# Kernel tuning notes

Hardware: AMD Instinct MI355X
Metric: run time of the kernel (lower is better)

The kernel has to match this reference:

```python
import jax, jax.numpy as jnp
import numpy as np
import math

N = 100000
D = 128      # input_dim
H = 4        # heads
DK = 32      # d_k
DV = D // H  # d_v = 32


def setup_inputs() -> dict:
    key = jax.random.key(0)
    k1, k2, k3, k4, k5 = jax.random.split(key, 5)
    x = jax.random.normal(k1, (N, D), dtype=jnp.float32)
    neighbor_index = jax.random.randint(k2, (N, 4), 0, N, dtype=jnp.int64)
    w_q = jax.random.normal(k3, (H, D, DK), dtype=jnp.float32) * 0.05
    w_k = jax.random.normal(k4, (H, 5, D, DK), dtype=jnp.float32) * 0.05
    w_v = jax.random.normal(k5, (H, 5, D, DV), dtype=jnp.float32) * 0.05
    return {"x": x, "neighbor_index": neighbor_index, "w_q": w_q, "w_k": w_k, "w_v": w_v}


def reference(x, neighbor_index, w_q, w_k, w_v):
    n = x.shape[0]
    d_k = w_q.shape[-1]
    # gather 4 neighbors, prepend self node -> (N, 5, D)
    x_neighbors = jnp.concatenate([x[:, None, :], x[neighbor_index]], axis=1)
    Q = jnp.einsum('nd,hdk->hnk', x, w_q)                 # (H, N, DK)
    K = jnp.einsum('nrd,hrdk->hnrk', x_neighbors, w_k)    # (H, N, 5, DK)
    V = jnp.einsum('nrd,hrdv->hnrv', x_neighbors, w_v)    # (H, N, 5, DV)
    A = jnp.einsum('hnk,hnrk->hnr', Q, K) / math.sqrt(d_k)
    # NOTE: original torch code applies softmax over dim=1, which is the NODE
    # dimension (not the neighbor dimension r). Replicated faithfully.
    A = jax.nn.softmax(A, axis=1)
    Z = jnp.einsum('hnr,hnrv->hnv', A, V)                 # (H, N, DV)
    return Z.transpose(1, 0, 2).reshape(n, -1)            # (N, H*DV)
```

## Files before the change

### kernel.cpp

```cpp
#include <hip/hip_runtime.h>


#define N_NODES 100000
#define D 128
#define H 4
#define R 5
#define NPB 64
#define THREADS 256
#define NBLOCKS ((N_NODES + NPB - 1) / NPB)

typedef _Float16 half_t;
typedef __attribute__((ext_vector_type(8))) _Float16 f16x8;
typedef __attribute__((ext_vector_type(4))) float f32x4;

typedef const __attribute__((address_space(1))) unsigned int* gp_t;
typedef __attribute__((address_space(3))) unsigned int* lp_t;

__device__ __forceinline__ void async_copy16(const void* g, void* l) {
    __builtin_amdgcn_global_load_lds((gp_t)g, (lp_t)l, 16, 0, 0);
}

__global__ void prep_x(const float* __restrict__ x, half_t* __restrict__ xh)
{
    const int total = N_NODES * D / 8;
    for (int i = blockIdx.x * blockDim.x + threadIdx.x; i < total;
         i += gridDim.x * blockDim.x) {
        const float4* s = (const float4*)x + (size_t)i * 2;
        float4 a = s[0], b = s[1];
        f16x8 h = {(half_t)a.x, (half_t)a.y, (half_t)a.z, (half_t)a.w,
                   (half_t)b.x, (half_t)b.y, (half_t)b.z, (half_t)b.w};
        *((f16x8*)xh + i) = h;
    }
}

__global__ void prep_w(const float* __restrict__ wq, const float* __restrict__ wk,
                       const float* __restrict__ wv, half_t* __restrict__ wph)
{
    const int m = blockIdx.x;
    const float* src = (m < 4) ? (wq + m * 4096)
                     : (m < 24) ? (wk + (m - 4) * 4096)
                                : (wv + (m - 24) * 4096);
    const int t = threadIdx.x;
#pragma unroll
    for (int i = 0; i < 16; ++i) {
        int p = t * 16 + i;
        int j = p & 7, ln = (p >> 3) & 63, f = p >> 9;
        int kt = f & 3, mt = f >> 2;
        int d = kt * 32 + (ln >> 4) * 8 + j;
        int ko = mt * 16 + (ln & 15);
        wph[m * 4096 + p] = (half_t)src[d * 32 + ko];
    }
}

__device__ __forceinline__ void stage_tile(const half_t* __restrict__ xh,
                                           const int* __restrict__ nbr,
                                           int base, int r, char* tile)
{
    const int w = threadIdx.x >> 6;
    const int lane = threadIdx.x & 63;
    const int rr = lane >> 4, c = lane & 15;
#pragma unroll
    for (int i = 0; i < 4; ++i) {
        int row0 = w * 16 + i * 4;
        int row = row0 + rr;
        int node = base + row;
        if (node >= N_NODES) node = N_NODES - 1;
        int src = (r == 0) ? node : nbr[node * 4 + (r - 1)];
        const char* g = (const char*)xh + (size_t)src * 256 + ((c ^ (row & 7)) << 4);
        async_copy16(g, tile + row0 * 256);
    }
}

__device__ __forceinline__ void proj(int mid, const half_t* __restrict__ wph,
                                     const half_t* tile, int lane,
                                     f32x4 (&acc)[2][4])
{
    const int l15 = lane & 15;
    const int q = lane >> 4;
#pragma unroll
    for (int mt = 0; mt < 2; ++mt)
#pragma unroll
        for (int nt = 0; nt < 4; ++nt)
            acc[mt][nt] = (f32x4){0.f, 0.f, 0.f, 0.f};

#pragma unroll
    for (int kt = 0; kt < 4; ++kt) {
        f16x8 a0 = *(const f16x8*)(wph + ((mid * 8 + kt) * 64 + lane) * 8);
        f16x8 a1 = *(const f16x8*)(wph + ((mid * 8 + 4 + kt) * 64 + lane) * 8);
#pragma unroll
        for (int nt = 0; nt < 4; ++nt) {
            int row = nt * 16 + l15;
            int sq = (kt * 4 + q) ^ (row & 7);
            f16x8 b = *(const f16x8*)(tile + row * 128 + sq * 8);
            acc[0][nt] = __builtin_amdgcn_mfma_f32_16x16x32_f16(a0, b, acc[0][nt], 0, 0, 0);
            acc[1][nt] = __builtin_amdgcn_mfma_f32_16x16x32_f16(a1, b, acc[1][nt], 0, 0, 0);
        }
    }
}

__global__ __launch_bounds__(THREADS, 3)
void knot_logits(const half_t* __restrict__ xh, const int* __restrict__ nbr,
                 const half_t* __restrict__ wph,
                 half_t* __restrict__ eh, float* __restrict__ sums_p)
{
    __shared__ __align__(16) char smem[NPB * 256];
    half_t* tile = (half_t*)smem;
    const int base = blockIdx.x * NPB;
    const int lane = threadIdx.x & 63;
    const int h = __builtin_amdgcn_readfirstlane((int)(threadIdx.x >> 6));
    const int l15 = lane & 15;

    stage_tile(xh, nbr, base, 0, smem);
    __syncthreads();

    f32x4 qf[2][4];
    proj(h, wph, tile, lane, qf);

    f32x4 kf[2][4];
#pragma unroll 1
    for (int r = 0; r < R; ++r) {
        if (r > 0) {
            __syncthreads();
            stage_tile(xh, nbr, base, r, smem);
            __syncthreads();
        }
        proj(4 + h * 5 + r, wph, tile, lane, kf);

        float esum = 0.f;
#pragma unroll
        for (int nt = 0; nt < 4; ++nt) {
            float p = 0.f;
#pragma unroll
            for (int mt = 0; mt < 2; ++mt)
#pragma unroll
                for (int j = 0; j < 4; ++j)
                    p += qf[mt][nt][j] * kf[mt][nt][j];
            p += __shfl_xor(p, 16, 64);
            p += __shfl_xor(p, 32, 64);
            int node = base + nt * 16 + l15;
            float e = (node < N_NODES) ? __expf(p * 0.17677669529663688f) : 0.f;
            if ((lane >> 4) == 0 && node < N_NODES)
                eh[(size_t)(h * 5 + r) * N_NODES + node] = (half_t)e;
            esum += e;
        }
        esum += __shfl_xor(esum, 1, 64);
        esum += __shfl_xor(esum, 2, 64);
        esum += __shfl_xor(esum, 4, 64);
        esum += __shfl_xor(esum, 8, 64);
        if (lane == 0)
            atomicAdd(&sums_p[(h * 5 + r) * 64 + (blockIdx.x & 63)], esum);
    }
}

__global__ void knot_reduce(const float* __restrict__ sums_p, float* __restrict__ sums)
{
    const int w = threadIdx.x >> 6;
    const int lane = threadIdx.x & 63;
#pragma unroll
    for (int i = 0; i < 5; ++i) {
        int hr = w * 5 + i;
        float v = sums_p[hr * 64 + lane];
        v += __shfl_xor(v, 1, 64);
        v += __shfl_xor(v, 2, 64);
        v += __shfl_xor(v, 4, 64);
        v += __shfl_xor(v, 8, 64);
        v += __shfl_xor(v, 16, 64);
        v += __shfl_xor(v, 32, 64);
        if (lane == 0) sums[hr] = v;
    }
}

#define VS 67
#define HS 2152
__global__ __launch_bounds__(THREADS, 3)
void knot_out(const half_t* __restrict__ xh, const int* __restrict__ nbr,
              const half_t* __restrict__ wph,
              const half_t* __restrict__ eh, const float* __restrict__ sums,
              float* __restrict__ out)
{
    __shared__ __align__(16) char smem[2 * HS * 4];
    half_t* tile = (half_t*)smem;
    const int base = blockIdx.x * NPB;
    const int lane = threadIdx.x & 63;
    const int h = __builtin_amdgcn_readfirstlane((int)(threadIdx.x >> 6));
    const int l15 = lane & 15;
    const int q = lane >> 4;

    f32x4 z[2][4];
#pragma unroll
    for (int mt = 0; mt < 2; ++mt)
#pragma unroll
        for (int nt = 0; nt < 4; ++nt)
            z[mt][nt] = (f32x4){0.f, 0.f, 0.f, 0.f};

    f32x4 vf[2][4];
#pragma unroll 1
    for (int r = 0; r < R; ++r) {
        if (r > 0) __syncthreads();
        stage_tile(xh, nbr, base, r, smem);
        __syncthreads();
        proj(24 + h * 5 + r, wph, tile, lane, vf);

        float inv = 1.0f / sums[h * 5 + r];
#pragma unroll
        for (int nt = 0; nt < 4; ++nt) {
            int node = base + nt * 16 + l15;
            if (node >= N_NODES) node = N_NODES - 1;
            float w = (float)eh[(size_t)(h * 5 + r) * N_NODES + node] * inv;
#pragma unroll
            for (int mt = 0; mt < 2; ++mt)
#pragma unroll
                for (int j = 0; j < 4; ++j)
                    z[mt][nt][j] += w * vf[mt][nt][j];
        }
    }

    __syncthreads();
    float* zt = (float*)smem;
#pragma unroll 1
    for (int pass = 0; pass < 2; ++pass) {
        if (pass) __syncthreads();
        if ((h >> 1) == pass) {
#pragma unroll
            for (int mt = 0; mt < 2; ++mt)
#pragma unroll
                for (int nt = 0; nt < 4; ++nt)
#pragma unroll
                    for (int j = 0; j < 4; ++j) {
                        int v = mt * 16 + q * 4 + j;
                        zt[(h & 1) * HS + v * VS + nt * 16 + l15] = z[mt][nt][j];
                    }
        }
        __syncthreads();
        const int row = threadIdx.x >> 2;
        const int c = threadIdx.x & 3;
        if (base + row < N_NODES) {
            float* dst = out + (size_t)(base + row) * D + pass * 64 + c * 16;
#pragma unroll
            for (int i4 = 0; i4 < 4; ++i4) {
                float4 v4;
#pragma unroll
                for (int e = 0; e < 4; ++e) {
                    int col = c * 16 + i4 * 4 + e;
                    int h2 = col >> 5, v = col & 31;
                    ((float*)&v4)[e] = zt[h2 * HS + v * VS + row];
                }
                *(float4*)(dst + i4 * 4) = v4;
            }
        }
    }
}

extern "C" void kernel_launch(void* const* d_in, const int* in_sizes, int n_in,
                              void* d_out, int out_size, void* d_ws, size_t ws_size,
                              hipStream_t stream)
{
    const float* x   = (const float*)d_in[0];
    const int*   nbr = (const int*)d_in[1];
    const float* w_q = (const float*)d_in[2];
    const float* w_k = (const float*)d_in[3];
    const float* w_v = (const float*)d_in[4];
    float* out = (float*)d_out;

    float*  sums   = (float*)d_ws;
    float*  sums_p = sums + 32;
    half_t* eh     = (half_t*)((char*)d_ws + 8192);
    half_t* wph    = (half_t*)((char*)d_ws + 4194304);
    half_t* xh     = (half_t*)((char*)d_ws + 4718592);

    hipMemsetAsync(d_ws, 0, 5248, stream);
    prep_x<<<2048, THREADS, 0, stream>>>(x, xh);
    prep_w<<<44, THREADS, 0, stream>>>(w_q, w_k, w_v, wph);
    knot_logits<<<NBLOCKS, THREADS, 0, stream>>>(xh, nbr, wph, eh, sums_p);
    knot_reduce<<<1, THREADS, 0, stream>>>(sums_p, sums);
    knot_out<<<NBLOCKS, THREADS, 0, stream>>>(xh, nbr, wph, eh, sums, out);
}
```

Baseline: 222.7 us.

## Double-buffer neighbor tiles, merge prep kernels, fold sum reduction into output kernel

Both the logits and output kernels now use two LDS buffers, so the gather of the next neighbor's rows is issued while MFMAs run on the current tile. Neighbor indices are loaded once per node as an int4, and the per-slot loop is unrolled at compile time. The two prep kernels become one launch, and the separate reduce kernel is removed by having each knot_out block reduce the partial sums itself. This cuts launches and sync stalls, at the cost of double the LDS per block (which may lower occupancy) and redundant per-block reduction work.

```diff
diff --git a/kernel.cpp b/kernel.cpp
--- a/kernel.cpp
+++ b/kernel.cpp
@@ -20,80 +20,92 @@
     __builtin_amdgcn_global_load_lds((gp_t)g, (lp_t)l, 16, 0, 0);
 }
 
-__global__ void prep_x(const float* __restrict__ x, half_t* __restrict__ xh)
-{
-    const int total = N_NODES * D / 8;
-    for (int i = blockIdx.x * blockDim.x + threadIdx.x; i < total;
-         i += gridDim.x * blockDim.x) {
-        const float4* s = (const float4*)x + (size_t)i * 2;
-        float4 a = s[0], b = s[1];
-        f16x8 h = {(half_t)a.x, (half_t)a.y, (half_t)a.z, (half_t)a.w,
-                   (half_t)b.x, (half_t)b.y, (half_t)b.z, (half_t)b.w};
-        *((f16x8*)xh + i) = h;
-    }
-}
-
-__global__ void prep_w(const float* __restrict__ wq, const float* __restrict__ wk,
-                       const float* __restrict__ wv, half_t* __restrict__ wph)
-{
-    const int m = blockIdx.x;
-    const float* src = (m < 4) ? (wq + m * 4096)
-                     : (m < 24) ? (wk + (m - 4) * 4096)
-                                : (wv + (m - 24) * 4096);
+template<int V> struct ic { static constexpr int value = V; };
+
+__global__ void prep(const float* __restrict__ x,
+                     const float* __restrict__ wq, const float* __restrict__ wk,
+                     const float* __restrict__ wv,
+                     half_t* __restrict__ xh, half_t* __restrict__ wph)
+{
+    const int bid = blockIdx.x;
     const int t = threadIdx.x;
-#pragma unroll
-    for (int i = 0; i < 16; ++i) {
-        int p = t * 16 + i;
-        int j = p & 7, ln = (p >> 3) & 63, f = p >> 9;
-        int kt = f & 3, mt = f >> 2;
-        int d = kt * 32 + (ln >> 4) * 8 + j;
-        int ko = mt * 16 + (ln & 15);
-        wph[m * 4096 + p] = (half_t)src[d * 32 + ko];
-    }
-}
-
-__device__ __forceinline__ void stage_tile(const half_t* __restrict__ xh,
-                                           const int* __restrict__ nbr,
-                                           int base, int r, char* tile)
-{
-    const int w = threadIdx.x >> 6;
-    const int lane = threadIdx.x & 63;
-    const int rr = lane >> 4, c = lane & 15;
+    if (bid < 44) {
+        const float* src = (bid < 4) ? (wq + bid * 4096)
+                         : (bid < 24) ? (wk + (bid - 4) * 4096)
+                                      : (wv + (bid - 24) * 4096);
+#pragma unroll
+        for (int i = 0; i < 16; ++i) {
+            int p = t * 16 + i;
+            int j = p & 7, ln = (p >> 3) & 63, f = p >> 9;
+            int kt = f & 3, mt = f >> 2;
+            int d = kt * 32 + (ln >> 4) * 8 + j;
+            int ko = mt * 16 + (ln & 15);
+            wph[bid * 4096 + p] = (half_t)src[d * 32 + ko];
+        }
+    } else {
+        const int total = N_NODES * D / 8;
+        const int nb = gridDim.x - 44;
+        for (int i = (bid - 44) * THREADS + t; i < total; i += nb * THREADS) {
+            const float4* s = (const float4*)x + (size_t)i * 2;
+            float4 a = s[0], b = s[1];
+            f16x8 h8 = {(half_t)a.x, (half_t)a.y, (half_t)a.z, (half_t)a.w,
+                        (half_t)b.x, (half_t)b.y, (half_t)b.z, (half_t)b.w};
+            *((f16x8*)xh + i) = h8;
+        }
+    }
+}
+
+template<int SLOT>
+__device__ __forceinline__ void stage_slot(const half_t* __restrict__ xh,
+                                           const int (&rows)[4], const int4 (&nb4)[4],
+                                           int base, char* buf, int lane)
+{
+    const int rr = lane >> 4;
+    const int c = lane & 15;
 #pragma unroll
     for (int i = 0; i < 4; ++i) {
-        int row0 = w * 16 + i * 4;
-        int row = row0 + rr;
-        int node = base + row;
-        if (node >= N_NODES) node = N_NODES - 1;
-        int src = (r == 0) ? node : nbr[node * 4 + (r - 1)];
+        int row = rows[i];
+        int src;
+        if constexpr (SLOT == 0) {
+            int node = base + row;
+            src = (node >= N_NODES) ? (N_NODES - 1) : node;
+        } else if constexpr (SLOT == 1) src = nb4[i].x;
+        else if constexpr (SLOT == 2) src = nb4[i].y;
+        else if constexpr (SLOT == 3) src = nb4[i].z;
+        else                          src = nb4[i].w;
         const char* g = (const char*)xh + (size_t)src * 256 + ((c ^ (row & 7)) << 4);
-        async_copy16(g, tile + row0 * 256);
-    }
-}
-
-__device__ __forceinline__ void proj(int mid, const half_t* __restrict__ wph,
-                                     const half_t* tile, int lane,
-                                     f32x4 (&acc)[2][4])
-{
-    const int l15 = lane & 15;
-    const int q = lane >> 4;
+        async_copy16(g, buf + (row - rr) * 256);
+    }
+}
+
+__device__ __forceinline__ void load_af(int mid, const half_t* __restrict__ wph,
+                                        int lane, f16x8 (&af)[8])
+{
+#pragma unroll
+    for (int kt = 0; kt < 4; ++kt) {
+        af[kt * 2]     = *(const f16x8*)(wph + ((mid * 8 + kt) * 64 + lane) * 8);
+        af[kt * 2 + 1] = *(const f16x8*)(wph + ((mid * 8 + 4 + kt) * 64 + lane) * 8);
+    }
+}
+
+__device__ __forceinline__ void proj_mfma(const f16x8 (&af)[8], const half_t* tile,
+                                          int lane, f32x4 (&acc)[2][4])
+{
+    const int l15 = lane & 15, q = lane >> 4;
 #pragma unroll
     for (int mt = 0; mt < 2; ++mt)
 #pragma unroll
         for (int nt = 0; nt < 4; ++nt)
             acc[mt][nt] = (f32x4){0.f, 0.f, 0.f, 0.f};
-
 #pragma unroll
     for (int kt = 0; kt < 4; ++kt) {
-        f16x8 a0 = *(const f16x8*)(wph + ((mid * 8 + kt) * 64 + lane) * 8);
-        f16x8 a1 = *(const f16x8*)(wph + ((mid * 8 + 4 + kt) * 64 + lane) * 8);
 #pragma unroll
         for (int nt = 0; nt < 4; ++nt) {
             int row = nt * 16 + l15;
             int sq = (kt * 4 + q) ^ (row & 7);
             f16x8 b = *(const f16x8*)(tile + row * 128 + sq * 8);
-            acc[0][nt] = __builtin_amdgcn_mfma_f32_16x16x32_f16(a0, b, acc[0][nt], 0, 0, 0);
-            acc[1][nt] = __builtin_amdgcn_mfma_f32_16x16x32_f16(a1, b, acc[1][nt], 0, 0, 0);
+            acc[0][nt] = __builtin_amdgcn_mfma_f32_16x16x32_f16(af[kt * 2], b, acc[0][nt], 0, 0, 0);
+            acc[1][nt] = __builtin_amdgcn_mfma_f32_16x16x32_f16(af[kt * 2 + 1], b, acc[1][nt], 0, 0, 0);
         }
     }
 }
@@ -103,28 +115,41 @@
                  const half_t* __restrict__ wph,
                  half_t* __restrict__ eh, float* __restrict__ sums_p)
 {
-    __shared__ __align__(16) char smem[NPB * 256];
-    half_t* tile = (half_t*)smem;
+    __shared__ __align__(16) char bufA[NPB * 256];
+    __shared__ __align__(16) char bufB[NPB * 256];
     const int base = blockIdx.x * NPB;
     const int lane = threadIdx.x & 63;
     const int h = __builtin_amdgcn_readfirstlane((int)(threadIdx.x >> 6));
-    const int l15 = lane & 15;
-
-    stage_tile(xh, nbr, base, 0, smem);
+    const int l15 = lane & 15, rr = lane >> 4;
+
+    int rows[4]; int4 nb4[4];
+#pragma unroll
+    for (int i = 0; i < 4; ++i) {
+        rows[i] = h * 16 + i * 4 + rr;
+        int node = base + rows[i];
+        if (node >= N_NODES) node = N_NODES - 1;
+        nb4[i] = ((const int4*)nbr)[node];
+    }
+
+    stage_slot<0>(xh, rows, nb4, base, bufA, lane);
+    stage_slot<1>(xh, rows, nb4, base, bufB, lane);
     __syncthreads();
 
-    f32x4 qf[2][4];
-    proj(h, wph, tile, lane, qf);
-
-    f32x4 kf[2][4];
-#pragma unroll 1
-    for (int r = 0; r < R; ++r) {
-        if (r > 0) {
-            __syncthreads();
-            stage_tile(xh, nbr, base, r, smem);
-            __syncthreads();
-        }
-        proj(4 + h * 5 + r, wph, tile, lane, kf);
+    f16x8 af[8];
+    f32x4 qf[2][4], kf[2][4];
+    load_af(h, wph, lane, af);
+    proj_mfma(af, (const half_t*)bufA, lane, qf);
+
+    auto slot = [&](auto rc) {
+        constexpr int r = decltype(rc)::value;
+        const half_t* cur = (const half_t*)((r & 1) ? bufB : bufA);
+        char* nxt = ((r + 1) & 1) ? bufB : bufA;
+        load_af(4 + h * 5 + r, wph, lane, af);
+        if constexpr (r >= 1 && r <= 3) {
+            __builtin_amdgcn_sched_barrier(0);
+            stage_slot<r + 1>(xh, rows, nb4, base, nxt, lane);
+        }
+        proj_mfma(af, cur, lane, kf);
 
         float esum = 0.f;
 #pragma unroll
@@ -139,7 +164,7 @@
             p += __shfl_xor(p, 32, 64);
             int node = base + nt * 16 + l15;
             float e = (node < N_NODES) ? __expf(p * 0.17677669529663688f) : 0.f;
-            if ((lane >> 4) == 0 && node < N_NODES)
+            if (rr == 0 && node < N_NODES)
                 eh[(size_t)(h * 5 + r) * N_NODES + node] = (half_t)e;
             esum += e;
         }
@@ -149,78 +174,95 @@
         esum += __shfl_xor(esum, 8, 64);
         if (lane == 0)
             atomicAdd(&sums_p[(h * 5 + r) * 64 + (blockIdx.x & 63)], esum);
-    }
-}
-
-__global__ void knot_reduce(const float* __restrict__ sums_p, float* __restrict__ sums)
-{
-    const int w = threadIdx.x >> 6;
-    const int lane = threadIdx.x & 63;
-#pragma unroll
-    for (int i = 0; i < 5; ++i) {
-        int hr = w * 5 + i;
-        float v = sums_p[hr * 64 + lane];
-        v += __shfl_xor(v, 1, 64);
-        v += __shfl_xor(v, 2, 64);
-        v += __shfl_xor(v, 4, 64);
-        v += __shfl_xor(v, 8, 64);
-        v += __shfl_xor(v, 16, 64);
-        v += __shfl_xor(v, 32, 64);
-        if (lane == 0) sums[hr] = v;
-    }
+        __syncthreads();
+    };
+    slot(ic<0>{}); slot(ic<1>{}); slot(ic<2>{}); slot(ic<3>{}); slot(ic<4>{});
 }
 
 #define VS 67
-#define HS 2152
 __global__ __launch_bounds__(THREADS, 3)
 void knot_out(const half_t* __restrict__ xh, const int* __restrict__ nbr,
-              const half_t* __restrict__ wph,
-              const half_t* __restrict__ eh, const float* __restrict__ sums,
-              float* __restrict__ out)
-{
-    __shared__ __align__(16) char smem[2 * HS * 4];
-    half_t* tile = (half_t*)smem;
+              const half_t* __restrict__ wph, const half_t* __restrict__ eh,
+              const float* __restrict__ sums_p, float* __restrict__ out)
+{
+    __shared__ __align__(16) char bufA[NPB * 256];
+    __shared__ __align__(16) char bufB[NPB * 256];
+    __shared__ float sums_s[20];
     const int base = blockIdx.x * NPB;
     const int lane = threadIdx.x & 63;
     const int h = __builtin_amdgcn_readfirstlane((int)(threadIdx.x >> 6));
-    const int l15 = lane & 15;
-    const int q = lane >> 4;
-
-    f32x4 z[2][4];
+    const int l15 = lane & 15, rr = lane >> 4, q = rr;
+
+#pragma unroll
+    for (int i = 0; i < 5; ++i) {
+        int hr = h * 5 + i;
+        float v = sums_p[hr * 64 + lane];
+        v += __shfl_xor(v, 1, 64);  v += __shfl_xor(v, 2, 64);
+        v += __shfl_xor(v, 4, 64);  v += __shfl_xor(v, 8, 64);
+        v += __shfl_xor(v, 16, 64); v += __shfl_xor(v, 32, 64);
+        if (lane == 0) sums_s[hr] = v;
+    }
+
+    int rows[4]; int4 nb4[4];
+#pragma unroll
+    for (int i = 0; i < 4; ++i) {
+        rows[i] = h * 16 + i * 4 + rr;
+        int node = base + rows[i];
+        if (node >= N_NODES) node = N_NODES - 1;
+        nb4[i] = ((const int4*)nbr)[node];
+    }
+
+    stage_slot<0>(xh, rows, nb4, base, bufA, lane);
+    stage_slot<1>(xh, rows, nb4, base, bufB, lane);
+    __syncthreads();
+
+    float inv[5];
+#pragma unroll
+    for (int r = 0; r < 5; ++r) inv[r] = 1.0f / sums_s[h * 5 + r];
+
+    f16x8 af[8];
+    f32x4 z[2][4], vf[2][4];
 #pragma unroll
     for (int mt = 0; mt < 2; ++mt)
 #pragma unroll
         for (int nt = 0; nt < 4; ++nt)
             z[mt][nt] = (f32x4){0.f, 0.f, 0.f, 0.f};
 
-    f32x4 vf[2][4];
-#pragma unroll 1
-    for (int r = 0; r < R; ++r) {
-        if (r > 0) __syncthreads();
-        stage_tile(xh, nbr, base, r, smem);
-        __syncthreads();
-        proj(24 + h * 5 + r, wph, tile, lane, vf);
-
-        float inv = 1.0f / sums[h * 5 + r];
+    auto slot = [&](auto rc) {
+        constexpr int r = decltype(rc)::value;
+        const half_t* cur = (const half_t*)((r & 1) ? bufB : bufA);
+        char* nxt = ((r + 1) & 1) ? bufB : bufA;
+        load_af(24 + h * 5 + r, wph, lane, af);
+        float ev[4];
 #pragma unroll
         for (int nt = 0; nt < 4; ++nt) {
             int node = base + nt * 16 + l15;
             if (node >= N_NODES) node = N_NODES - 1;
-            float w = (float)eh[(size_t)(h * 5 + r) * N_NODES + node] * inv;
+            ev[nt] = (float)eh[(size_t)(h * 5 + r) * N_NODES + node];
+        }
+        if constexpr (r >= 1 && r <= 3) {
+            __builtin_amdgcn_sched_barrier(0);
+            stage_slot<r + 1>(xh, rows, nb4, base, nxt, lane);
+        }
+        proj_mfma(af, cur, lane, vf);
+#pragma unroll
+        for (int nt = 0; nt < 4; ++nt) {
+            float w = ev[nt] * inv[r];
 #pragma unroll
             for (int mt = 0; mt < 2; ++mt)
 #pragma unroll
                 for (int j = 0; j < 4; ++j)
                     z[mt][nt][j] += w * vf[mt][nt][j];
         }
-    }
-
-    __syncthreads();
-    float* zt = (float*)smem;
+        __syncthreads();
+    };
+    slot(ic<0>{}); slot(ic<1>{}); slot(ic<2>{}); slot(ic<3>{}); slot(ic<4>{});
+
 #pragma unroll 1
     for (int pass = 0; pass < 2; ++pass) {
         if (pass) __syncthreads();
         if ((h >> 1) == pass) {
+            float* ztp = (float*)((h & 1) ? bufB : bufA);
 #pragma unroll
             for (int mt = 0; mt < 2; ++mt)
 #pragma unroll
@@ -228,7 +270,7 @@
 #pragma unroll
                     for (int j = 0; j < 4; ++j) {
                         int v = mt * 16 + q * 4 + j;
-                        zt[(h & 1) * HS + v * VS + nt * 16 + l15] = z[mt][nt][j];
+                        ztp[v * VS + nt * 16 + l15] = z[mt][nt][j];
                     }
         }
         __syncthreads();
@@ -242,8 +284,8 @@
 #pragma unroll
                 for (int e = 0; e < 4; ++e) {
                     int col = c * 16 + i4 * 4 + e;
-                    int h2 = col >> 5, v = col & 31;
-                    ((float*)&v4)[e] = zt[h2 * HS + v * VS + row];
+                    const float* ztp = (const float*)((col & 32) ? bufB : bufA);
+                    ((float*)&v4)[e] = ztp[(col & 31) * VS + row];
                 }
                 *(float4*)(dst + i4 * 4) = v4;
             }
@@ -262,16 +304,13 @@
     const float* w_v = (const float*)d_in[4];
     float* out = (float*)d_out;
 
-    float*  sums   = (float*)d_ws;
-    float*  sums_p = sums + 32;
+    float*  sums_p = (float*)d_ws;
     half_t* eh     = (half_t*)((char*)d_ws + 8192);
     half_t* wph    = (half_t*)((char*)d_ws + 4194304);
     half_t* xh     = (half_t*)((char*)d_ws + 4718592);
 
-    hipMemsetAsync(d_ws, 0, 5248, stream);
-    prep_x<<<2048, THREADS, 0, stream>>>(x, xh);
-    prep_w<<<44, THREADS, 0, stream>>>(w_q, w_k, w_v, wph);
+    hipMemsetAsync(d_ws, 0, 5120, stream);
+    prep<<<44 + 2048, THREADS, 0, stream>>>(x, w_q, w_k, w_v, xh, wph);
     knot_logits<<<NBLOCKS, THREADS, 0, stream>>>(xh, nbr, wph, eh, sums_p);
-    knot_reduce<<<1, THREADS, 0, stream>>>(sums_p, sums);
-    knot_out<<<NBLOCKS, THREADS, 0, stream>>>(xh, nbr, wph, eh, sums, out);
-}
+    knot_out<<<NBLOCKS, THREADS, 0, stream>>>(xh, nbr, wph, eh, sums_p, out);
+}
```

Result: faster. 205.6 us (-7.7%).
